# Kernel tuning notes

Hardware: AMD Instinct MI355X
Metric: run time of the kernel (lower is better)

Reference implementation:

```python
import jax, jax.numpy as jnp
import numpy as np

NEG_SLOPE = 0.2

def _segment_softmax(logits, seg, num_segments):
    m = jax.ops.segment_max(logits, seg, num_segments=num_segments)
    m = jnp.where(jnp.isfinite(m), m, 0.0)
    e = jnp.exp(logits - m[seg])
    s = jax.ops.segment_sum(e, seg, num_segments=num_segments)
    return e / (s[seg] + 1e-16)

def _gat_conv(x, src, dst, W, att_src, att_dst, b):
    # PyG GATConv, heads=1, concat=True, add_self_loops=True
    N = x.shape[0]
    h = x @ W                                   # [N, C]
    a_src = h @ att_src                         # [N]
    a_dst = h @ att_dst                         # [N]
    loop = jnp.arange(N, dtype=src.dtype)
    s = jnp.concatenate([src, loop])            # add self-loops
    d = jnp.concatenate([dst, loop])
    logits = jax.nn.leaky_relu(a_src[s] + a_dst[d], NEG_SLOPE)  # [E+N]
    w = _segment_softmax(logits, d, N)
    out = jax.ops.segment_sum(h[s] * w[:, None], d, num_segments=N)
    return out + b

def _sage_conv(x, src, dst, W_l, W_r, b):
    # PyG SAGEConv, aggr='mean', root_weight=True, normalize=False
    N = x.shape[0]
    agg = jax.ops.segment_sum(x[src], dst, num_segments=N)      # [N, C]
    deg = jax.ops.segment_sum(jnp.ones_like(src, dtype=x.dtype), dst, num_segments=N)
    mean = agg / jnp.maximum(deg, 1.0)[:, None]
    return mean @ W_l + x @ W_r + b

def setup_inputs() -> dict:
    key = jax.random.key(0)
    ks = jax.random.split(key, 12)
    N, E, EL, F_IN, D = 100000, 1000000, 200000, 11, 64
    glorot = lambda k, sh: jax.random.uniform(k, sh, jnp.float32, -1.0, 1.0) * np.sqrt(6.0 / (sh[0] + sh[-1]))
    return {
        "x": jax.random.normal(ks[0], (N, F_IN), jnp.float32),
        "edge_index": jax.random.randint(ks[1], (2, E), 0, N, jnp.int64),
        "edge_label_index": jax.random.randint(ks[2], (2, EL), 0, N, jnp.int64),
        "W_gat": glorot(ks[3], (F_IN, D)),
        "att_src": glorot(ks[4], (D,)),
        "att_dst": glorot(ks[5], (D,)),
        "b_gat": jnp.zeros((D,), jnp.float32),
        "W1_l": glorot(ks[6], (D, D)),
        "W1_r": glorot(ks[7], (D, D)),
        "b1": jnp.zeros((D,), jnp.float32),
        "W2_l": glorot(ks[8], (D, D)),
        "W2_r": glorot(ks[9], (D, D)),
        "b2": jnp.zeros((D,), jnp.float32),
        "alpha": jnp.full((4,), 1.0 / 4.0, jnp.float32),  # num_layers + 1
    }

def reference(x, edge_index, edge_label_index, W_gat, att_src, att_dst, b_gat,
              W1_l, W1_r, b1, W2_l, W2_r, b2, alpha):
    src, dst = edge_index[0], edge_index[1]
    weights = jax.nn.softmax(alpha)
    # Faithful to original get_embedding (note: weights[1] is skipped, as in source)
    h = _gat_conv(x, src, dst, W_gat, att_src, att_dst, b_gat)
    out = h * weights[0]
    h = _sage_conv(h, src, dst, W1_l, W1_r, b1)
    out = out + h * weights[2]
    h = _sage_conv(h, src, dst, W2_l, W2_r, b2)
    out = out + h * weights[3]
    # link prediction: gather + elementwise dot
    return (out[edge_label_index[0]] * out[edge_label_index[1]]).sum(-1)
```

## Files before the change

### kernel.cpp

```cpp
#include <hip/hip_runtime.h>
#include <math.h>
#include <float.h>

#define NEG_SLOPE 0.2f
#define NCHUNK 256

typedef _Float16 half8 __attribute__((ext_vector_type(8)));
typedef float f32x4  __attribute__((ext_vector_type(4)));

__global__ __launch_bounds__(256) void gat_input_kernel(
    const float* __restrict__ x, const float* __restrict__ Wg,
    const float* __restrict__ att_src, const float* __restrict__ att_dst,
    _Float16* __restrict__ Hf, float* __restrict__ a_src, float* __restrict__ a_dst, int N,
    const float* __restrict__ W1l, const float* __restrict__ W1r,
    const float* __restrict__ W2l, const float* __restrict__ W2r,
    _Float16* __restrict__ W1hi, _Float16* __restrict__ W1lo,
    _Float16* __restrict__ W2hi, _Float16* __restrict__ W2lo,
    const float* __restrict__ alpha, float* __restrict__ wsm,
    _Float16* __restrict__ HG, _Float16* __restrict__ H1)
{
    __shared__ float Wl[11 * 64];
    int tid = threadIdx.x;

    if (blockIdx.x < 8) {
        if (blockIdx.x == 0 && tid == 0) {
            float m = alpha[0];
            for (int i = 1; i < 4; i++) m = fmaxf(m, alpha[i]);
            float e[4], s = 0.f;
            for (int i = 0; i < 4; i++) { e[i] = expf(alpha[i] - m); s += e[i]; }
            for (int i = 0; i < 4; i++) wsm[i] = e[i] / s;
        }
        int which = blockIdx.x >> 2;
        const float* Wlp = which ? W2l : W1l;
        const float* Wrp = which ? W2r : W1r;
        _Float16* Whi = which ? W2hi : W1hi;
        _Float16* Wlo = which ? W2lo : W1lo;
        int idx = (blockIdx.x & 3) * 256 + tid;
        int kc = idx >> 8, rem = idx & 255;
        int t = rem >> 6, ln = rem & 63;
        int quad = ln >> 4, col16 = ln & 15;
        int c = t * 16 + col16;
        #pragma unroll
        for (int j = 0; j < 8; j++) {
            int k = kc * 32 + quad * 8 + j;
            float w = (k < 64) ? Wlp[k * 64 + c] : Wrp[(k - 64) * 64 + c];
            _Float16 hi = (_Float16)w;
            _Float16 lo = (_Float16)(w - (float)hi);
            Whi[(size_t)idx * 8 + j] = hi;
            Wlo[(size_t)idx * 8 + j] = lo;
        }
    } else if (blockIdx.x == 8) {
        if (tid < 64) Hf[(size_t)N * 64 + tid] = (_Float16)0.f;
        else if (tid < 128) HG[(size_t)N * 64 + (tid - 64)] = (_Float16)0.f;
        else if (tid < 192) H1[(size_t)N * 64 + (tid - 128)] = (_Float16)0.f;
        else if (tid == 192) a_src[N] = -1e30f;
    }

    for (int i = tid; i < 11 * 64; i += 256) Wl[i] = Wg[i];
    __syncthreads();
    int lane = tid & 63;
    int n = blockIdx.x * 4 + (tid >> 6);
    if (n >= N) return;
    float xv = (lane < 11) ? x[n * 11 + lane] : 0.f;
    float acc = 0.f;
    #pragma unroll
    for (int k = 0; k < 11; k++) acc += __shfl(xv, k, 64) * Wl[k * 64 + lane];
    Hf[(size_t)n * 64 + lane] = (_Float16)acc;
    float ps = acc * att_src[lane];
    float pd = acc * att_dst[lane];
    for (int off = 32; off; off >>= 1) {
        ps += __shfl_down(ps, off, 64);
        pd += __shfl_down(pd, off, 64);
    }
    if (lane == 0) { a_src[n] = ps; a_dst[n] = pd; }
}


__global__ __launch_bounds__(1024) void edge_hist_kernel(
    const int* __restrict__ dst, int* __restrict__ hist, int E, int NBK)
{
    __shared__ int c[1024];
    int t = threadIdx.x;
    c[t] = 0;
    __syncthreads();
    int chunk = (E + NCHUNK - 1) / NCHUNK;
    int lo = blockIdx.x * chunk;
    int hi = lo + chunk; if (hi > E) hi = E;
    for (int i = lo + t; i < hi; i += 1024)
        atomicAdd(&c[dst[i] >> 7], 1);
    __syncthreads();
    if (t < NBK) hist[t * NCHUNK + blockIdx.x] = c[t];
}

__global__ __launch_bounds__(256) void scan_reduce_kernel(
    const int* __restrict__ v, int* __restrict__ bsum, int M)
{
    __shared__ int s[256];
    int t = threadIdx.x;
    int base = blockIdx.x * 1024 + t * 4;
    int sum = 0;
    #pragma unroll
    for (int j = 0; j < 4; j++) { int idx = base + j; if (idx < M) sum += v[idx]; }
    s[t] = sum; __syncthreads();
    for (int off = 128; off; off >>= 1) {
        if (t < off) s[t] += s[t + off];
        __syncthreads();
    }
    if (t == 0) bsum[blockIdx.x] = s[0];
}

__global__ __launch_bounds__(256) void scan_apply_kernel(
    const int* __restrict__ v, const int* __restrict__ bsum,
    int* __restrict__ out, int M, int NB)
{
    __shared__ int s[256];
    int t = threadIdx.x;
    int bv = (t < NB) ? bsum[t] : 0;
    s[t] = bv; __syncthreads();
    for (int off = 1; off < 256; off <<= 1) {
        int xx = (t >= off) ? s[t - off] : 0;
        __syncthreads();
        s[t] += xx;
        __syncthreads();
    }
    int blockoff = (blockIdx.x == 0) ? 0 : s[blockIdx.x - 1];
    __syncthreads();
    int base = blockIdx.x * 1024;
    int vv[4]; int sum = 0;
    #pragma unroll
    for (int j = 0; j < 4; j++) {
        int idx = base + t * 4 + j;
        vv[j] = (idx < M) ? v[idx] : 0;
        sum += vv[j];
    }
    s[t] = sum; __syncthreads();
    for (int off = 1; off < 256; off <<= 1) {
        int xx = (t >= off) ? s[t - off] : 0;
        __syncthreads();
        s[t] += xx;
        __syncthreads();
    }
    int ex = s[t] - sum + blockoff;
    #pragma unroll
    for (int j = 0; j < 4; j++) {
        int idx = base + t * 4 + j;
        if (idx < M) out[idx] = ex;
        ex += vv[j];
    }
}

__global__ __launch_bounds__(1024) void edge_scatter_kernel(
    const int* __restrict__ src, const int* __restrict__ dst,
    const int* __restrict__ rstart, unsigned* __restrict__ ebuf, int E, int NBK)
{
    __shared__ int cur[1024];
    int t = threadIdx.x;
    if (t < NBK) cur[t] = rstart[t * NCHUNK + blockIdx.x];
    __syncthreads();
    int chunk = (E + NCHUNK - 1) / NCHUNK;
    int lo = blockIdx.x * chunk;
    int hi = lo + chunk; if (hi > E) hi = E;
    for (int i = lo + t; i < hi; i += 1024) {
        int d = dst[i];
        int p = atomicAdd(&cur[d >> 7], 1);
        ebuf[p] = ((unsigned)src[i] << 7) | (unsigned)(d & 127);
    }
}

__global__ __launch_bounds__(256) void bucket_build_kernel(
    const unsigned* __restrict__ ebuf, const int* __restrict__ rstart,
    int* __restrict__ cnt, int* __restrict__ rowstart,
    int* __restrict__ csr, int E, int N, int NBK)
{
    __shared__ int c[128];
    __shared__ int rs[128];
    __shared__ int cur[128];
    int b = blockIdx.x, t = threadIdx.x;
    if (t < 128) { c[t] = 0; cur[t] = 0; }
    __syncthreads();
    int beg = rstart[b * NCHUNK];
    int end = (b == NBK - 1) ? E : rstart[(b + 1) * NCHUNK];
    int n = end - beg;
    int pbeg = beg + 384 * b;
    for (int j = t; j < n; j += 256)
        atomicAdd(&c[ebuf[beg + j] & 127u], 1);
    __syncthreads();
    int myc = (t < 128) ? c[t] : 0;
    int mypc = (myc + 3) & ~3;
    if (t < 128) rs[t] = mypc;
    __syncthreads();
    for (int off = 1; off < 128; off <<= 1) {
        int v = (t < 128 && t >= off) ? rs[t - off] : 0;
        __syncthreads();
        if (t < 128) rs[t] += v;
        __syncthreads();
    }
    int ex = (t < 128) ? (rs[t] - mypc) : 0;
    __syncthreads();
    if (t < 128) rs[t] = ex;
    int base = b << 7;
    if (t < 128 && base + t < N) {
        cnt[base + t] = myc;
        rowstart[base + t] = pbeg + ex;
    }
    __syncthreads();
    for (int j = t; j < n; j += 256) {
        unsigned e = ebuf[beg + j];
        int d = (int)(e & 127u);
        int p = atomicAdd(&cur[d], 1);
        csr[pbeg + rs[d] + p] = (int)(e >> 7);
    }
    __syncthreads();
    if (t < 128) {
        for (int k = myc; k < mypc; k++) csr[pbeg + rs[t] + k] = N;
    }
}

__global__ __launch_bounds__(256) void gat_gather_kernel(
    const _Float16* __restrict__ Hf, const float* __restrict__ a_src,
    const float* __restrict__ a_dst, const float* __restrict__ bg,
    const int* __restrict__ rowstart, const int* __restrict__ cnt,
    const int* __restrict__ csr, const float* __restrict__ wsm,
    _Float16* __restrict__ HG, _Float16* __restrict__ outD, int N)
{
    const half8* __restrict__ H8 = (const half8*)Hf;
    int tid = threadIdx.x;
    int lane = tid & 63;
    int g = lane >> 3, sub = lane & 7;
    int gl = g << 3;
    int d = blockIdx.x * 32 + (tid >> 3);
    if (d >= N) return;
    float ad = a_dst[d];
    int beg = rowstart[d], deg = cnt[d];
    int degp = (deg + 3) & ~3;
    float a0 = a_src[d] + ad;
    float lg0 = a0 > 0.f ? a0 : NEG_SLOPE * a0;
    float w_self = expf(lg0);
    half8 hself = H8[(size_t)d * 8 + sub];
    float acc[8];
    #pragma unroll
    for (int c = 0; c < 8; c++) acc[c] = w_self * (float)hself[c];
    float l_lane = 0.f;
    for (int base = 0; base < degp; base += 16) {
        int sidA = (base + sub < degp) ? csr[beg + base + sub] : N;
        float aaA = a_src[sidA] + ad;
        float lgA = aaA > 0.f ? aaA : NEG_SLOPE * aaA;
        float wA = expf(lgA);
        l_lane += wA;
        if (degp - base > 8) {
            int sidB = (base + 8 + sub < degp) ? csr[beg + base + 8 + sub] : N;
            float aaB = a_src[sidB] + ad;
            float lgB = aaB > 0.f ? aaB : NEG_SLOPE * aaB;
            float wB = expf(lgB);
            l_lane += wB;
            int ib[16]; float wb[16];
            #pragma unroll
            for (int j = 0; j < 8; j++) {
                ib[j]     = __shfl(sidA, gl + j, 64);
                wb[j]     = __shfl(wA,   gl + j, 64);
                ib[8 + j] = __shfl(sidB, gl + j, 64);
                wb[8 + j] = __shfl(wB,   gl + j, 64);
            }
            half8 v[16];
            #pragma unroll
            for (int j = 0; j < 16; j++) v[j] = H8[(size_t)ib[j] * 8 + sub];
            #pragma unroll
            for (int j = 0; j < 16; j++) {
                #pragma unroll
                for (int c = 0; c < 8; c++) acc[c] += wb[j] * (float)v[j][c];
            }
        } else {
            int ib[8]; float wb[8];
            #pragma unroll
            for (int j = 0; j < 8; j++) {
                ib[j] = __shfl(sidA, gl + j, 64);
                wb[j] = __shfl(wA,   gl + j, 64);
            }
            half8 v[8];
            #pragma unroll
            for (int j = 0; j < 8; j++) v[j] = H8[(size_t)ib[j] * 8 + sub];
            #pragma unroll
            for (int j = 0; j < 8; j++) {
                #pragma unroll
                for (int c = 0; c < 8; c++) acc[c] += wb[j] * (float)v[j][c];
            }
        }
    }
    #pragma unroll
    for (int off = 1; off < 8; off <<= 1) l_lane += __shfl_xor(l_lane, off, 64);
    float l = l_lane + w_self;
    float inv = 1.0f / (l + 1e-16f);
    float w0s = wsm[0];
    size_t idx = (size_t)d * 8 + sub;
    half8 hg, od;
    #pragma unroll
    for (int c = 0; c < 8; c++) {
        float o = acc[c] * inv + bg[sub * 8 + c];
        hg[c] = (_Float16)o;
        od[c] = (_Float16)(w0s * o);
    }
    ((half8*)HG)[idx] = hg;
    ((half8*)outD)[idx] = od;
}

__global__ __launch_bounds__(256) void sage_fused_kernel(
    const _Float16* __restrict__ Hin,
    const _Float16* __restrict__ Whi, const _Float16* __restrict__ Wlo,
    const float* __restrict__ bvec,
    const int* __restrict__ rowstart, const int* __restrict__ cnt,
    const int* __restrict__ csr, const float* __restrict__ wsm, int widx,
    _Float16* __restrict__ hout, _Float16* __restrict__ outD, int N)
{
    __shared__ __align__(16) char smem[64 * 68 * 4];
    float* Ot = (float*)smem;
    const half8* __restrict__ H8 = (const half8*)Hin;
    int tid = threadIdx.x;
    int lane = tid & 63;
    int nodeBase = blockIdx.x * 64;
    int sub = tid & 7;
    int g = lane >> 3;
    int gl = g << 3;

    #pragma unroll
    for (int pass = 0; pass < 2; pass++) {
        int dloc = pass * 32 + (tid >> 3);
        int d = nodeBase + dloc;
        float acc[8];
        #pragma unroll
        for (int c = 0; c < 8; c++) acc[c] = 0.f;
        half8 hself;
        #pragma unroll
        for (int c = 0; c < 8; c++) hself[c] = (_Float16)0.f;
        float invd = 0.f;
        if (d < N) {
            int beg = rowstart[d], deg = cnt[d];
            int degp = (deg + 3) & ~3;
            for (int base2 = 0; base2 < degp; base2 += 16) {
                int sidA = (base2 + sub < degp) ? csr[beg + base2 + sub] : N;
                if (degp - base2 > 8) {
                    int sidB = (base2 + 8 + sub < degp) ? csr[beg + base2 + 8 + sub] : N;
                    int ib[16];
                    #pragma unroll
                    for (int j = 0; j < 8; j++) {
                        ib[j]     = __shfl(sidA, gl + j, 64);
                        ib[8 + j] = __shfl(sidB, gl + j, 64);
                    }
                    half8 v[16];
                    #pragma unroll
                    for (int j = 0; j < 16; j++) v[j] = H8[(size_t)ib[j] * 8 + sub];
                    #pragma unroll
                    for (int j = 0; j < 16; j++) {
                        #pragma unroll
                        for (int c = 0; c < 8; c++) acc[c] += (float)v[j][c];
                    }
                } else {
                    int ib[8];
                    #pragma unroll
                    for (int j = 0; j < 8; j++) ib[j] = __shfl(sidA, gl + j, 64);
                    half8 v[8];
                    #pragma unroll
                    for (int j = 0; j < 8; j++) v[j] = H8[(size_t)ib[j] * 8 + sub];
                    #pragma unroll
                    for (int j = 0; j < 8; j++) {
                        #pragma unroll
                        for (int c = 0; c < 8; c++) acc[c] += (float)v[j][c];
                    }
                }
            }
            invd = 1.0f / fmaxf((float)deg, 1.0f);
            hself = H8[(size_t)d * 8 + sub];
        }
        half8 ah;
        #pragma unroll
        for (int c = 0; c < 8; c++) ah[c] = (_Float16)(acc[c] * invd);
        int rbase = dloc * 256;
        int swz = (dloc & 7) << 4;
        *(half8*)(smem + ((rbase + sub * 16) ^ swz)) = ah;
        *(half8*)(smem + ((rbase + 128 + sub * 16) ^ swz)) = hself;
    }
    __syncthreads();

    int quad = lane >> 4, col16 = lane & 15;
    int wave = tid >> 6;
    int row = wave * 16 + col16;
    int rswz = (row & 7) << 4;
    f32x4 accq[4];
    #pragma unroll
    for (int t = 0; t < 4; t++) accq[t] = (f32x4){0.f, 0.f, 0.f, 0.f};
    #pragma unroll
    for (int kc = 0; kc < 4; kc++) {
        half8 av = *(const half8*)(smem + ((row * 256 + kc * 64 + quad * 16) ^ rswz));
        #pragma unroll
        for (int t = 0; t < 4; t++) {
            size_t off = (size_t)((kc * 4 + t) * 64 + lane) * 8;
            half8 bhi = *(const half8*)(Whi + off);
            half8 blo = *(const half8*)(Wlo + off);
            accq[t] = __builtin_amdgcn_mfma_f32_16x16x32_f16(av, bhi, accq[t], 0, 0, 0);
            accq[t] = __builtin_amdgcn_mfma_f32_16x16x32_f16(av, blo, accq[t], 0, 0, 0);
        }
    }
    __syncthreads();
    #pragma unroll
    for (int t = 0; t < 4; t++) {
        #pragma unroll
        for (int r = 0; r < 4; r++) {
            Ot[(wave * 16 + quad * 4 + r) * 68 + t * 16 + col16] = accq[t][r];
        }
    }
    __syncthreads();

    float w = wsm[widx];
    #pragma unroll
    for (int pass = 0; pass < 2; pass++) {
        int dloc = pass * 32 + (tid >> 3);
        int d = nodeBase + dloc;
        if (d >= N) continue;
        size_t idx = (size_t)d * 8 + sub;
        float4 o0 = *(float4*)&Ot[dloc * 68 + sub * 8];
        float4 o1 = *(float4*)&Ot[dloc * 68 + sub * 8 + 4];
        float4 b0 = *(const float4*)&bvec[sub * 8];
        float4 b1v = *(const float4*)&bvec[sub * 8 + 4];
        float o[8] = {o0.x + b0.x, o0.y + b0.y, o0.z + b0.z, o0.w + b0.w,
                      o1.x + b1v.x, o1.y + b1v.y, o1.z + b1v.z, o1.w + b1v.w};
        half8 od = ((half8*)outD)[idx];
        half8 ho;
        #pragma unroll
        for (int c = 0; c < 8; c++) {
            ho[c] = (_Float16)o[c];
            od[c] = (_Float16)((float)od[c] + w * o[c]);
        }
        if (hout) ((half8*)hout)[idx] = ho;
        ((half8*)outD)[idx] = od;
    }
}

__global__ __launch_bounds__(256) void link_pred_kernel(
    const int* __restrict__ eli, const _Float16* __restrict__ outf,
    float* __restrict__ out, int EL)
{
    const half8* __restrict__ o8 = (const half8*)outf;
    int grp = (threadIdx.x >> 3);
    int sub = threadIdx.x & 7;
    int e0 = blockIdx.x * 64 + grp;
    int e1 = e0 + 32;
    int a0 = 0, b0 = 0, a1 = 0, b1 = 0;
    bool v0 = e0 < EL, v1 = e1 < EL;
    if (v0) { a0 = eli[e0]; b0 = eli[EL + e0]; }
    if (v1) { a1 = eli[e1]; b1 = eli[EL + e1]; }
    float p0 = 0.f, p1 = 0.f;
    if (v0) {
        half8 pa = o8[(size_t)a0 * 8 + sub];
        half8 pb = o8[(size_t)b0 * 8 + sub];
        #pragma unroll
        for (int c = 0; c < 8; c++) p0 += (float)pa[c] * (float)pb[c];
    }
    if (v1) {
        half8 pa = o8[(size_t)a1 * 8 + sub];
        half8 pb = o8[(size_t)b1 * 8 + sub];
        #pragma unroll
        for (int c = 0; c < 8; c++) p1 += (float)pa[c] * (float)pb[c];
    }
    for (int off = 4; off; off >>= 1) {
        p0 += __shfl_xor(p0, off, 64);
        p1 += __shfl_xor(p1, off, 64);
    }
    if (sub == 0) {
        if (v0) out[e0] = p0;
        if (v1) out[e1] = p1;
    }
}

extern "C" void kernel_launch(void* const* d_in, const int* in_sizes, int n_in,
                              void* d_out, int out_size, void* d_ws, size_t ws_size,
                              hipStream_t stream)
{
    const float* x      = (const float*)d_in[0];
    const int*   ei     = (const int*)d_in[1];
    const int*   eli    = (const int*)d_in[2];
    const float* Wg     = (const float*)d_in[3];
    const float* att_s  = (const float*)d_in[4];
    const float* att_d  = (const float*)d_in[5];
    const float* bg     = (const float*)d_in[6];
    const float* W1l    = (const float*)d_in[7];
    const float* W1r    = (const float*)d_in[8];
    const float* b1     = (const float*)d_in[9];
    const float* W2l    = (const float*)d_in[10];
    const float* W2r    = (const float*)d_in[11];
    const float* b2     = (const float*)d_in[12];
    const float* alpha  = (const float*)d_in[13];

    const int N  = in_sizes[0] / 11;
    const int E  = in_sizes[1] / 2;
    const int EL = in_sizes[2] / 2;
    const int NBK = (N + 127) >> 7;
    const int M   = NBK * NCHUNK;
    const int NB  = (M + 1023) / 1024;
    const int CSRSZ = E + 384 * NBK;

    const int* src = ei;
    const int* dst = ei + E;

    _Float16* Hf  = (_Float16*)d_ws;
    _Float16* HG  = Hf + (size_t)(N + 1) * 64;
    _Float16* H1  = HG + (size_t)(N + 1) * 64;
    _Float16* oD  = H1 + (size_t)(N + 1) * 64;
    _Float16* wf  = oD + (size_t)N * 64;
    _Float16* W1hi = wf;
    _Float16* W1lo = wf + 8192;
    _Float16* W2hi = wf + 16384;
    _Float16* W2lo = wf + 24576;
    float* wsm     = (float*)(wf + 32768);
    float* a_src   = wsm + 4;
    float* a_dst   = a_src + (N + 1);
    int*   cnt     = (int*)(a_dst + N);
    int*   rowstart= cnt + N;
    int*   hist    = rowstart + N;
    int*   rstart  = hist + M;
    int*   bsum    = rstart + M;
    int*   csr     = bsum + 256;
    unsigned* ebuf = (unsigned*)(csr + CSRSZ);

    gat_input_kernel<<<(N + 3) / 4, 256, 0, stream>>>(x, Wg, att_s, att_d, Hf,
                                                      a_src, a_dst, N,
                                                      W1l, W1r, W2l, W2r,
                                                      W1hi, W1lo, W2hi, W2lo,
                                                      alpha, wsm, HG, H1);
    edge_hist_kernel<<<NCHUNK, 1024, 0, stream>>>(dst, hist, E, NBK);
    scan_reduce_kernel<<<NB, 256, 0, stream>>>(hist, bsum, M);
    scan_apply_kernel<<<NB, 256, 0, stream>>>(hist, bsum, rstart, M, NB);
    edge_scatter_kernel<<<NCHUNK, 1024, 0, stream>>>(src, dst, rstart, ebuf, E, NBK);
    bucket_build_kernel<<<NBK, 256, 0, stream>>>(ebuf, rstart, cnt, rowstart, csr, E, N, NBK);
    gat_gather_kernel<<<(N + 31) / 32, 256, 0, stream>>>(Hf, a_src, a_dst, bg,
                                                         rowstart, cnt, csr, wsm, HG, oD, N);
    sage_fused_kernel<<<(N + 63) / 64, 256, 0, stream>>>(HG, W1hi, W1lo, b1,
                                                         rowstart, cnt, csr, wsm, 2, H1, oD, N);
    sage_fused_kernel<<<(N + 63) / 64, 256, 0, stream>>>(H1, W2hi, W2lo, b2,
                                                         rowstart, cnt, csr, wsm, 3, nullptr, oD, N);
    link_pred_kernel<<<(EL + 63) / 64, 256, 0, stream>>>(eli, oD, (float*)d_out, EL);
}
```

Before: 251.3 us.

## Build CSR with direct per-node global atomics instead of two-level bucket sort

Replaces the bucketed histogram/scatter/bucket-build CSR construction with a simple per-destination count via global atomics, a scan over padded node degrees, and a global-atomic scatter of sources. This drops the intermediate ebuf pass and the per-bucket build kernel, and zeroes counts inside the input kernel. In exchange it relies on many contended global atomics with random access, and edges within a row now land in nondeterministic order.

```diff
diff --git a/kernel.cpp b/kernel.cpp
--- a/kernel.cpp
+++ b/kernel.cpp
@@ -3,7 +3,6 @@
 #include <float.h>
 
 #define NEG_SLOPE 0.2f
-#define NCHUNK 256
 
 typedef _Float16 half8 __attribute__((ext_vector_type(8)));
 typedef float f32x4  __attribute__((ext_vector_type(4)));
@@ -17,10 +16,16 @@
     _Float16* __restrict__ W1hi, _Float16* __restrict__ W1lo,
     _Float16* __restrict__ W2hi, _Float16* __restrict__ W2lo,
     const float* __restrict__ alpha, float* __restrict__ wsm,
-    _Float16* __restrict__ HG, _Float16* __restrict__ H1)
+    _Float16* __restrict__ HG, _Float16* __restrict__ H1,
+    int* __restrict__ cnt)
 {
     __shared__ float Wl[11 * 64];
     int tid = threadIdx.x;
+
+    {
+        int zi = blockIdx.x * 256 + tid;
+        if (zi < N) cnt[zi] = 0;
+    }
 
     if (blockIdx.x < 8) {
         if (blockIdx.x == 0 && tid == 0) {
@@ -76,31 +81,25 @@
 }
 
 
-__global__ __launch_bounds__(1024) void edge_hist_kernel(
-    const int* __restrict__ dst, int* __restrict__ hist, int E, int NBK)
-{
-    __shared__ int c[1024];
-    int t = threadIdx.x;
-    c[t] = 0;
-    __syncthreads();
-    int chunk = (E + NCHUNK - 1) / NCHUNK;
-    int lo = blockIdx.x * chunk;
-    int hi = lo + chunk; if (hi > E) hi = E;
-    for (int i = lo + t; i < hi; i += 1024)
-        atomicAdd(&c[dst[i] >> 7], 1);
-    __syncthreads();
-    if (t < NBK) hist[t * NCHUNK + blockIdx.x] = c[t];
+__global__ __launch_bounds__(1024) void edge_count_kernel(
+    const int* __restrict__ dst, int* __restrict__ cnt, int E)
+{
+    int i = blockIdx.x * 1024 + threadIdx.x;
+    if (i < E) atomicAdd(&cnt[dst[i]], 1);
 }
 
 __global__ __launch_bounds__(256) void scan_reduce_kernel(
-    const int* __restrict__ v, int* __restrict__ bsum, int M)
+    const int* __restrict__ cnt, int* __restrict__ bsum, int N)
 {
     __shared__ int s[256];
     int t = threadIdx.x;
     int base = blockIdx.x * 1024 + t * 4;
     int sum = 0;
     #pragma unroll
-    for (int j = 0; j < 4; j++) { int idx = base + j; if (idx < M) sum += v[idx]; }
+    for (int j = 0; j < 4; j++) {
+        int idx = base + j;
+        if (idx < N) sum += (cnt[idx] + 3) & ~3;
+    }
     s[t] = sum; __syncthreads();
     for (int off = 128; off; off >>= 1) {
         if (t < off) s[t] += s[t + off];
@@ -110,8 +109,9 @@
 }
 
 __global__ __launch_bounds__(256) void scan_apply_kernel(
-    const int* __restrict__ v, const int* __restrict__ bsum,
-    int* __restrict__ out, int M, int NB)
+    const int* __restrict__ cnt, const int* __restrict__ bsum,
+    int* __restrict__ rowstart, int* __restrict__ cur,
+    int* __restrict__ csr, int N, int NB)
 {
     __shared__ int s[256];
     int t = threadIdx.x;
@@ -126,11 +126,13 @@
     int blockoff = (blockIdx.x == 0) ? 0 : s[blockIdx.x - 1];
     __syncthreads();
     int base = blockIdx.x * 1024;
-    int vv[4]; int sum = 0;
+    int vv[4], dg[4]; int sum = 0;
     #pragma unroll
     for (int j = 0; j < 4; j++) {
         int idx = base + t * 4 + j;
-        vv[j] = (idx < M) ? v[idx] : 0;
+        int c = (idx < N) ? cnt[idx] : 0;
+        dg[j] = c;
+        vv[j] = (c + 3) & ~3;
         sum += vv[j];
     }
     s[t] = sum; __syncthreads();
@@ -144,75 +146,23 @@
     #pragma unroll
     for (int j = 0; j < 4; j++) {
         int idx = base + t * 4 + j;
-        if (idx < M) out[idx] = ex;
+        if (idx < N) {
+            rowstart[idx] = ex;
+            cur[idx] = ex;
+            for (int k = dg[j]; k < vv[j]; k++) csr[ex + k] = N;
+        }
         ex += vv[j];
     }
 }
 
 __global__ __launch_bounds__(1024) void edge_scatter_kernel(
     const int* __restrict__ src, const int* __restrict__ dst,
-    const int* __restrict__ rstart, unsigned* __restrict__ ebuf, int E, int NBK)
-{
-    __shared__ int cur[1024];
-    int t = threadIdx.x;
-    if (t < NBK) cur[t] = rstart[t * NCHUNK + blockIdx.x];
-    __syncthreads();
-    int chunk = (E + NCHUNK - 1) / NCHUNK;
-    int lo = blockIdx.x * chunk;
-    int hi = lo + chunk; if (hi > E) hi = E;
-    for (int i = lo + t; i < hi; i += 1024) {
-        int d = dst[i];
-        int p = atomicAdd(&cur[d >> 7], 1);
-        ebuf[p] = ((unsigned)src[i] << 7) | (unsigned)(d & 127);
-    }
-}
-
-__global__ __launch_bounds__(256) void bucket_build_kernel(
-    const unsigned* __restrict__ ebuf, const int* __restrict__ rstart,
-    int* __restrict__ cnt, int* __restrict__ rowstart,
-    int* __restrict__ csr, int E, int N, int NBK)
-{
-    __shared__ int c[128];
-    __shared__ int rs[128];
-    __shared__ int cur[128];
-    int b = blockIdx.x, t = threadIdx.x;
-    if (t < 128) { c[t] = 0; cur[t] = 0; }
-    __syncthreads();
-    int beg = rstart[b * NCHUNK];
-    int end = (b == NBK - 1) ? E : rstart[(b + 1) * NCHUNK];
-    int n = end - beg;
-    int pbeg = beg + 384 * b;
-    for (int j = t; j < n; j += 256)
-        atomicAdd(&c[ebuf[beg + j] & 127u], 1);
-    __syncthreads();
-    int myc = (t < 128) ? c[t] : 0;
-    int mypc = (myc + 3) & ~3;
-    if (t < 128) rs[t] = mypc;
-    __syncthreads();
-    for (int off = 1; off < 128; off <<= 1) {
-        int v = (t < 128 && t >= off) ? rs[t - off] : 0;
-        __syncthreads();
-        if (t < 128) rs[t] += v;
-        __syncthreads();
-    }
-    int ex = (t < 128) ? (rs[t] - mypc) : 0;
-    __syncthreads();
-    if (t < 128) rs[t] = ex;
-    int base = b << 7;
-    if (t < 128 && base + t < N) {
-        cnt[base + t] = myc;
-        rowstart[base + t] = pbeg + ex;
-    }
-    __syncthreads();
-    for (int j = t; j < n; j += 256) {
-        unsigned e = ebuf[beg + j];
-        int d = (int)(e & 127u);
-        int p = atomicAdd(&cur[d], 1);
-        csr[pbeg + rs[d] + p] = (int)(e >> 7);
-    }
-    __syncthreads();
-    if (t < 128) {
-        for (int k = myc; k < mypc; k++) csr[pbeg + rs[t] + k] = N;
+    int* __restrict__ cur, int* __restrict__ csr, int E)
+{
+    int i = blockIdx.x * 1024 + threadIdx.x;
+    if (i < E) {
+        int p = atomicAdd(&cur[dst[i]], 1);
+        csr[p] = src[i];
     }
 }
 
@@ -492,10 +442,9 @@
     const int N  = in_sizes[0] / 11;
     const int E  = in_sizes[1] / 2;
     const int EL = in_sizes[2] / 2;
-    const int NBK = (N + 127) >> 7;
-    const int M   = NBK * NCHUNK;
-    const int NB  = (M + 1023) / 1024;
-    const int CSRSZ = E + 384 * NBK;
+    const int NB  = (N + 1023) / 1024;
+    const int EB  = (E + 1023) / 1024;
+    const int CSRSZ = E + 3 * N + 16;
 
     const int* src = ei;
     const int* dst = ei + E;
@@ -514,22 +463,19 @@
     float* a_dst   = a_src + (N + 1);
     int*   cnt     = (int*)(a_dst + N);
     int*   rowstart= cnt + N;
-    int*   hist    = rowstart + N;
-    int*   rstart  = hist + M;
-    int*   bsum    = rstart + M;
+    int*   cur     = rowstart + N;
+    int*   bsum    = cur + N;
     int*   csr     = bsum + 256;
-    unsigned* ebuf = (unsigned*)(csr + CSRSZ);
 
     gat_input_kernel<<<(N + 3) / 4, 256, 0, stream>>>(x, Wg, att_s, att_d, Hf,
                                                       a_src, a_dst, N,
                                                       W1l, W1r, W2l, W2r,
                                                       W1hi, W1lo, W2hi, W2lo,
-                                                      alpha, wsm, HG, H1);
-    edge_hist_kernel<<<NCHUNK, 1024, 0, stream>>>(dst, hist, E, NBK);
-    scan_reduce_kernel<<<NB, 256, 0, stream>>>(hist, bsum, M);
-    scan_apply_kernel<<<NB, 256, 0, stream>>>(hist, bsum, rstart, M, NB);
-    edge_scatter_kernel<<<NCHUNK, 1024, 0, stream>>>(src, dst, rstart, ebuf, E, NBK);
-    bucket_build_kernel<<<NBK, 256, 0, stream>>>(ebuf, rstart, cnt, rowstart, csr, E, N, NBK);
+                                                      alpha, wsm, HG, H1, cnt);
+    edge_count_kernel<<<EB, 1024, 0, stream>>>(dst, cnt, E);
+    scan_reduce_kernel<<<NB, 256, 0, stream>>>(cnt, bsum, N);
+    scan_apply_kernel<<<NB, 256, 0, stream>>>(cnt, bsum, rowstart, cur, csr, N, NB);
+    edge_scatter_kernel<<<EB, 1024, 0, stream>>>(src, dst, cur, csr, E);
     gat_gather_kernel<<<(N + 31) / 32, 256, 0, stream>>>(Hf, a_src, a_dst, bg,
                                                          rowstart, cnt, csr, wsm, HG, oD, N);
     sage_fused_kernel<<<(N + 63) / 64, 256, 0, stream>>>(HG, W1hi, W1lo, b1,
```

Result: slower. 327.3 us (+30.3%).
